# Kernel tuning notes

Measured on AMD Instinct MI355X. Metric: run time of the kernel, lower is better.

Reference implementation:

```python
import jax, jax.numpy as jnp
import numpy as np

NUM_POINTS = 200000
IN_FEATURES = 128
OUT_FEATURES = 128
NUM_RELATIONS = 128
NUM_BLOCKS = 16
IN_BLOCK = IN_FEATURES // NUM_BLOCKS   # 8
OUT_BLOCK = OUT_FEATURES // NUM_BLOCKS  # 8


def setup_inputs() -> dict:
    key = jax.random.key(0)
    k1, k2, k3 = jax.random.split(key, 3)
    x = jax.random.normal(k1, (NUM_POINTS, IN_FEATURES), dtype=jnp.float32)
    # glorot-uniform init of the per-relation block-diagonal weights
    blocks = jax.nn.initializers.glorot_uniform()(
        k2, (NUM_RELATIONS, NUM_BLOCKS, IN_BLOCK, OUT_BLOCK), jnp.float32)
    rel = jax.random.randint(k3, (NUM_POINTS,), 0, NUM_RELATIONS)
    return {"x": x, "blocks": blocks, "rel": rel}


def reference(x, blocks, rel):
    # x: [p, num_blocks*in_block]; blocks: [R, nb, ib, ob]; rel: [p] int
    p = x.shape[0]
    R, nb, ib, ob = blocks.shape
    x_by_block = x.reshape(p, nb, ib)                 # [p, nb, ib]
    relation_blocks = blocks[rel]                     # gather: [p, nb, ib, ob]
    transformed = jnp.einsum('pnio,pni->pno', relation_blocks, x_by_block)
    return transformed.reshape(p, nb * ob)            # [p, out_features]
```

## Files before the change

kernel.cpp:

```cpp
#include <hip/hip_runtime.h>


__global__ __launch_bounds__(1024) void k_fused(
    const float* __restrict__ x, const float* __restrict__ w,
    const int* __restrict__ rel, float* __restrict__ out, int npoints)
{
    __shared__ float4 wlds[4][128][16];

    const int q = blockIdx.x >> 6;
    const int b = blockIdx.x & 63;

    const float4* wsrc = reinterpret_cast<const float4*>(w);
    #pragma unroll
    for (int j = 0; j < 8; ++j) {
        int f  = threadIdx.x + j * 1024;
        int r  = f >> 6;
        int lo = f & 63;
        int nl = lo >> 4;
        int k  = f & 15;
        wlds[nl][r][k ^ (r & 15)] = wsrc[r * 256 + q * 64 + lo];
    }
    __syncthreads();

    const int nl = threadIdx.x & 3;
    const int pt = threadIdx.x >> 2;
    const int chunk = (npoints + 63) >> 6;
    const int plo = b * chunk;
    const int phi = min(plo + chunk, npoints);
    const int n  = q * 4 + nl;

    int p = plo + pt;
    if (p >= phi) return;

    const float* xb = x + n * 8;
    float*       ob = out + n * 8;

    int r = rel[p];
    const float4* xv = reinterpret_cast<const float4*>(xb + (size_t)p * 128);
    float4 x0 = xv[0], x1 = xv[1];

    while (true) {
        int pn = p + 256;
        int pc = pn < phi ? pn : (phi - 1);
        int rn = rel[pc];
        const float4* xnv = reinterpret_cast<const float4*>(xb + (size_t)pc * 128);
        float4 xn0 = xnv[0], xn1 = xnv[1];

        const int s = r & 15;
        const float4* wr = wlds[nl][r];
        float xf[8] = {x0.x, x0.y, x0.z, x0.w, x1.x, x1.y, x1.z, x1.w};
        float a0 = 0.f, a1 = 0.f, a2 = 0.f, a3 = 0.f;
        float a4 = 0.f, a5 = 0.f, a6 = 0.f, a7 = 0.f;
        #pragma unroll
        for (int i = 0; i < 8; ++i) {
            float4 wA = wr[(2 * i)     ^ s];
            float4 wB = wr[(2 * i + 1) ^ s];
            float xi = xf[i];
            a0 = fmaf(xi, wA.x, a0);
            a1 = fmaf(xi, wA.y, a1);
            a2 = fmaf(xi, wA.z, a2);
            a3 = fmaf(xi, wA.w, a3);
            a4 = fmaf(xi, wB.x, a4);
            a5 = fmaf(xi, wB.y, a5);
            a6 = fmaf(xi, wB.z, a6);
            a7 = fmaf(xi, wB.w, a7);
        }
        float4* ov = reinterpret_cast<float4*>(ob + (size_t)p * 128);
        ov[0] = make_float4(a0, a1, a2, a3);
        ov[1] = make_float4(a4, a5, a6, a7);

        if (pn >= phi) break;
        p = pn; r = rn; x0 = xn0; x1 = xn1;
    }
}

__global__ __launch_bounds__(256) void brl_kernel(
    const float* __restrict__ x, const float* __restrict__ w,
    const int* __restrict__ rel, float* __restrict__ out, int npoints)
{
    int tid = blockIdx.x * 256 + threadIdx.x;
    int p = tid >> 4;
    if (p >= npoints) return;
    int n = tid & 15;
    int r = rel[p];
    const float4* xv = reinterpret_cast<const float4*>(x + (size_t)p * 128 + n * 8);
    float4 x0 = xv[0], x1 = xv[1];
    float xf[8] = {x0.x, x0.y, x0.z, x0.w, x1.x, x1.y, x1.z, x1.w};
    const float4* wv = reinterpret_cast<const float4*>(w + ((size_t)r * 16 + n) * 64);
    float acc[8] = {0.f, 0.f, 0.f, 0.f, 0.f, 0.f, 0.f, 0.f};
    #pragma unroll
    for (int i = 0; i < 8; ++i) {
        float4 w0 = wv[2 * i], w1 = wv[2 * i + 1];
        float wf[8] = {w0.x, w0.y, w0.z, w0.w, w1.x, w1.y, w1.z, w1.w};
        #pragma unroll
        for (int o = 0; o < 8; ++o) acc[o] = fmaf(xf[i], wf[o], acc[o]);
    }
    float4* ov = reinterpret_cast<float4*>(out + (size_t)p * 128 + n * 8);
    ov[0] = make_float4(acc[0], acc[1], acc[2], acc[3]);
    ov[1] = make_float4(acc[4], acc[5], acc[6], acc[7]);
}

extern "C" void kernel_launch(void* const* d_in, const int* in_sizes, int n_in,
                              void* d_out, int out_size, void* d_ws, size_t ws_size,
                              hipStream_t stream) {
    const float* x   = (const float*)d_in[0];
    const float* w   = (const float*)d_in[1];
    const int*   rel = (const int*)d_in[2];
    float*       out = (float*)d_out;

    int npoints = in_sizes[2];
    int R = in_sizes[1] / 1024;

    if (R == 128 && in_sizes[0] == npoints * 128) {
        k_fused<<<256, 1024, 0, stream>>>(x, w, rel, out, npoints);
    } else {
        int total = npoints * 16;
        brl_kernel<<<(total + 255) / 256, 256, 0, stream>>>(x, w, rel, out, npoints);
    }
}
```

Baseline: 198.2 us.

## Deepen prefetch to two iterations and interleave LDS weight layout across blocks

Prefetches x rows and relation indices two iterations ahead instead of one, so more global loads are in flight per thread to hide memory latency. It also reorganises the LDS weight table so the four n-blocks of a relation are interleaved within one 64-entry row with a 6-bit XOR swizzle, aiming to reduce bank conflicts among neighbouring threads that read different blocks. The cost is higher register pressure from the extra prefetched data and more complex address arithmetic.

```diff
diff --git a/kernel.cpp b/kernel.cpp
--- a/kernel.cpp
+++ b/kernel.cpp
@@ -5,7 +5,7 @@
     const float* __restrict__ x, const float* __restrict__ w,
     const int* __restrict__ rel, float* __restrict__ out, int npoints)
 {
-    __shared__ float4 wlds[4][128][16];
+    __shared__ float4 wlds[128][64];
 
     const int q = blockIdx.x >> 6;
     const int b = blockIdx.x & 63;
@@ -18,7 +18,7 @@
         int lo = f & 63;
         int nl = lo >> 4;
         int k  = f & 15;
-        wlds[nl][r][k ^ (r & 15)] = wsrc[r * 256 + q * 64 + lo];
+        wlds[r][((k << 2) | nl) ^ (r & 63)] = wsrc[r * 256 + q * 64 + lo];
     }
     __syncthreads();
 
@@ -29,48 +29,63 @@
     const int phi = min(plo + chunk, npoints);
     const int n  = q * 4 + nl;
 
-    int p = plo + pt;
-    if (p >= phi) return;
+    int p1 = plo + pt;
+    if (p1 >= phi) return;
 
     const float* xb = x + n * 8;
     float*       ob = out + n * 8;
 
-    int r = rel[p];
-    const float4* xv = reinterpret_cast<const float4*>(xb + (size_t)p * 128);
-    float4 x0 = xv[0], x1 = xv[1];
+    int r1 = rel[p1];
+    const float4* xv1 = reinterpret_cast<const float4*>(xb + (size_t)p1 * 128);
+    float4 xa1 = xv1[0], xb1 = xv1[1];
+
+    int p2 = p1 + 256;
+    int p2c = p2 < phi ? p2 : phi - 1;
+    int r2 = rel[p2c];
+    const float4* xv2 = reinterpret_cast<const float4*>(xb + (size_t)p2c * 128);
+    float4 xa2 = xv2[0], xb2 = xv2[1];
 
     while (true) {
-        int pn = p + 256;
-        int pc = pn < phi ? pn : (phi - 1);
-        int rn = rel[pc];
-        const float4* xnv = reinterpret_cast<const float4*>(xb + (size_t)pc * 128);
-        float4 xn0 = xnv[0], xn1 = xnv[1];
+        int p3 = p1 + 512;
+        int p3c = p3 < phi ? p3 : phi - 1;
+        int r3 = rel[p3c];
+        const float4* xv3 = reinterpret_cast<const float4*>(xb + (size_t)p3c * 128);
+        float4 xa3 = xv3[0], xb3 = xv3[1];
 
-        const int s = r & 15;
-        const float4* wr = wlds[nl][r];
-        float xf[8] = {x0.x, x0.y, x0.z, x0.w, x1.x, x1.y, x1.z, x1.w};
-        float a0 = 0.f, a1 = 0.f, a2 = 0.f, a3 = 0.f;
-        float a4 = 0.f, a5 = 0.f, a6 = 0.f, a7 = 0.f;
-        #pragma unroll
-        for (int i = 0; i < 8; ++i) {
-            float4 wA = wr[(2 * i)     ^ s];
-            float4 wB = wr[(2 * i + 1) ^ s];
-            float xi = xf[i];
-            a0 = fmaf(xi, wA.x, a0);
-            a1 = fmaf(xi, wA.y, a1);
-            a2 = fmaf(xi, wA.z, a2);
-            a3 = fmaf(xi, wA.w, a3);
-            a4 = fmaf(xi, wB.x, a4);
-            a5 = fmaf(xi, wB.y, a5);
-            a6 = fmaf(xi, wB.z, a6);
-            a7 = fmaf(xi, wB.w, a7);
+        {
+            const int s   = r1 & 63;
+            const int sHi = s & 0x38;
+            const int low = nl ^ (s & 3);
+            const float4* base = wlds[r1];
+            const float4* wrA = base + ((s & 4) | low);
+            const float4* wrB = base + (((s & 4) ^ 4) | low);
+            float xf[8] = {xa1.x, xa1.y, xa1.z, xa1.w,
+                           xb1.x, xb1.y, xb1.z, xb1.w};
+            float a0 = 0.f, a1 = 0.f, a2 = 0.f, a3 = 0.f;
+            float a4 = 0.f, a5 = 0.f, a6 = 0.f, a7 = 0.f;
+            #pragma unroll
+            for (int i = 0; i < 8; ++i) {
+                int off = (i << 3) ^ sHi;
+                float4 wA = wrA[off];
+                float4 wB = wrB[off];
+                float xi = xf[i];
+                a0 = fmaf(xi, wA.x, a0);
+                a1 = fmaf(xi, wA.y, a1);
+                a2 = fmaf(xi, wA.z, a2);
+                a3 = fmaf(xi, wA.w, a3);
+                a4 = fmaf(xi, wB.x, a4);
+                a5 = fmaf(xi, wB.y, a5);
+                a6 = fmaf(xi, wB.z, a6);
+                a7 = fmaf(xi, wB.w, a7);
+            }
+            float4* ov = reinterpret_cast<float4*>(ob + (size_t)p1 * 128);
+            ov[0] = make_float4(a0, a1, a2, a3);
+            ov[1] = make_float4(a4, a5, a6, a7);
         }
-        float4* ov = reinterpret_cast<float4*>(ob + (size_t)p * 128);
-        ov[0] = make_float4(a0, a1, a2, a3);
-        ov[1] = make_float4(a4, a5, a6, a7);
 
-        if (pn >= phi) break;
-        p = pn; r = rn; x0 = xn0; x1 = xn1;
+        if (p2 >= phi) break;
+        p1 = p2;  r1 = r2; xa1 = xa2; xb1 = xb2;
+        p2 = p3;  r2 = r3; xa2 = xa3; xb2 = xb3;
     }
 }
 
```

Result: no change. 197.3 us (-0.4%).

## Split each block's outputs across lane pairs with DPP exchange and deeper prefetch

Applied to the files above, without the earlier changes.

Each thread now computes four outputs of a block instead of eight. Lane pairs each load one float4 of x and exchange halves through a DPP quad-permute swap. The LDS weight layout is reorganised to [relation][64] with a new XOR swizzle. Loads are prefetched two iterations ahead, and each wavefront handles eight contiguous points per step, which should give more coalesced 128-byte row segments and more memory-level parallelism. In exchange it doubles the thread count per point and adds the DPP traffic and extra index arithmetic.

```diff
diff --git a/kernel.cpp b/kernel.cpp
--- a/kernel.cpp
+++ b/kernel.cpp
@@ -1,11 +1,21 @@
 #include <hip/hip_runtime.h>
 
+
+__device__ __forceinline__ float4 dpp_swap1(float4 v) {
+    union { float4 f; int i[4]; } a, b;
+    a.f = v;
+    b.i[0] = __builtin_amdgcn_update_dpp(0, a.i[0], 0xB1, 0xF, 0xF, true);
+    b.i[1] = __builtin_amdgcn_update_dpp(0, a.i[1], 0xB1, 0xF, 0xF, true);
+    b.i[2] = __builtin_amdgcn_update_dpp(0, a.i[2], 0xB1, 0xF, 0xF, true);
+    b.i[3] = __builtin_amdgcn_update_dpp(0, a.i[3], 0xB1, 0xF, 0xF, true);
+    return b.f;
+}
 
 __global__ __launch_bounds__(1024) void k_fused(
     const float* __restrict__ x, const float* __restrict__ w,
     const int* __restrict__ rel, float* __restrict__ out, int npoints)
 {
-    __shared__ float4 wlds[4][128][16];
+    __shared__ float4 wlds[128][64];
 
     const int q = blockIdx.x >> 6;
     const int b = blockIdx.x & 63;
@@ -18,59 +28,70 @@
         int lo = f & 63;
         int nl = lo >> 4;
         int k  = f & 15;
-        wlds[nl][r][k ^ (r & 15)] = wsrc[r * 256 + q * 64 + lo];
+        wlds[r][((k << 2) | nl) ^ (r & 63)] = wsrc[r * 256 + q * 64 + lo];
     }
     __syncthreads();
 
-    const int nl = threadIdx.x & 3;
-    const int pt = threadIdx.x >> 2;
+    const int lane = threadIdx.x & 63;
+    const int wv   = threadIdx.x >> 6;
+    const int pt8  = lane >> 3;
+    const int j    = lane & 7;
+    const int nl   = j >> 1;
+    const int h    = j & 1;
+
     const int chunk = (npoints + 63) >> 6;
     const int plo = b * chunk;
     const int phi = min(plo + chunk, npoints);
-    const int n  = q * 4 + nl;
 
-    int p = plo + pt;
-    if (p >= phi) return;
+    int g1 = plo + wv * 8;
+    if (g1 >= phi) return;
 
-    const float* xb = x + n * 8;
-    float*       ob = out + n * 8;
+    const float4* xv = reinterpret_cast<const float4*>(x) + q * 8 + j;
+    float4*       ov = reinterpret_cast<float4*>(out) + q * 8 + j;
 
-    int r = rel[p];
-    const float4* xv = reinterpret_cast<const float4*>(xb + (size_t)p * 128);
-    float4 x0 = xv[0], x1 = xv[1];
+    int p1  = g1 + pt8;
+    int p1c = min(p1, phi - 1);
+    int r1  = rel[p1c];
+    float4 xa1 = xv[(size_t)p1c * 32];
+
+    int g2  = g1 + 128;
+    int p2c = min(g2 + pt8, phi - 1);
+    int r2  = rel[p2c];
+    float4 xa2 = xv[(size_t)p2c * 32];
 
     while (true) {
-        int pn = p + 256;
-        int pc = pn < phi ? pn : (phi - 1);
-        int rn = rel[pc];
-        const float4* xnv = reinterpret_cast<const float4*>(xb + (size_t)pc * 128);
-        float4 xn0 = xnv[0], xn1 = xnv[1];
+        int g3  = g1 + 256;
+        int p3c = min(g3 + pt8, phi - 1);
+        int r3  = rel[p3c];
+        float4 xa3 = xv[(size_t)p3c * 32];
 
-        const int s = r & 15;
-        const float4* wr = wlds[nl][r];
-        float xf[8] = {x0.x, x0.y, x0.z, x0.w, x1.x, x1.y, x1.z, x1.w};
-        float a0 = 0.f, a1 = 0.f, a2 = 0.f, a3 = 0.f;
-        float a4 = 0.f, a5 = 0.f, a6 = 0.f, a7 = 0.f;
-        #pragma unroll
-        for (int i = 0; i < 8; ++i) {
-            float4 wA = wr[(2 * i)     ^ s];
-            float4 wB = wr[(2 * i + 1) ^ s];
-            float xi = xf[i];
-            a0 = fmaf(xi, wA.x, a0);
-            a1 = fmaf(xi, wA.y, a1);
-            a2 = fmaf(xi, wA.z, a2);
-            a3 = fmaf(xi, wA.w, a3);
-            a4 = fmaf(xi, wB.x, a4);
-            a5 = fmaf(xi, wB.y, a5);
-            a6 = fmaf(xi, wB.z, a6);
-            a7 = fmaf(xi, wB.w, a7);
+        {
+            float4 xo  = dpp_swap1(xa1);
+            float4 xlo = h ? xo  : xa1;
+            float4 xhi = h ? xa1 : xo;
+            const int s   = r1 & 63;
+            const int thi = s & 0x38;
+            const int t0  = ((h << 2) | nl) ^ (s & 7);
+            const float4* base = wlds[r1];
+            float xf[8] = {xlo.x, xlo.y, xlo.z, xlo.w,
+                           xhi.x, xhi.y, xhi.z, xhi.w};
+            float a0 = 0.f, a1 = 0.f, a2 = 0.f, a3 = 0.f;
+            #pragma unroll
+            for (int i = 0; i < 8; ++i) {
+                float4 wv4 = base[((i << 3) ^ thi) | t0];
+                float xi = xf[i];
+                a0 = fmaf(xi, wv4.x, a0);
+                a1 = fmaf(xi, wv4.y, a1);
+                a2 = fmaf(xi, wv4.z, a2);
+                a3 = fmaf(xi, wv4.w, a3);
+            }
+            if (p1 < phi)
+                ov[(size_t)p1 * 32] = make_float4(a0, a1, a2, a3);
         }
-        float4* ov = reinterpret_cast<float4*>(ob + (size_t)p * 128);
-        ov[0] = make_float4(a0, a1, a2, a3);
-        ov[1] = make_float4(a4, a5, a6, a7);
 
-        if (pn >= phi) break;
-        p = pn; r = rn; x0 = xn0; x1 = xn1;
+        if (g2 >= phi) break;
+        g1 = g2; p1 = g1 + pt8; r1 = r2; xa1 = xa2;
+        g2 = g3;                r2 = r3; xa2 = xa3;
     }
 }
 
```

Result: faster. 190.5 us (-3.9%).
